# Kernel tuning notes

Hardware: AMD Instinct MI355X
Metric: run time of the kernel (lower is better)

Reference implementation:

```python
import jax, jax.numpy as jnp
import numpy as np

B, L, V, D = 8, 1024, 64, 64  # num_vars == d_model required by the module's g*h broadcast
EPS = 1e-5


def _layer_norm(x, gamma, beta):
    mu = jnp.mean(x, axis=-1, keepdims=True)
    var = jnp.mean(jnp.square(x - mu), axis=-1, keepdims=True)
    return (x - mu) * jax.lax.rsqrt(var + EPS) * gamma + beta


def setup_inputs() -> dict:
    key = jax.random.key(0)
    ks = jax.random.split(key, 20)
    s = 0.05
    inp = {
        'x': jax.random.normal(ks[0], (B, L, V), jnp.float32),
        # per-variable GRN(1, D, D) params, batched over V
        'W1': jax.random.normal(ks[1], (V, D), jnp.float32) * s,   # lin1 weight [in=1 -> D]
        'b1': jax.random.normal(ks[2], (V, D), jnp.float32) * s,
        'W2': jax.random.normal(ks[3], (V, D, D), jnp.float32) * s,
        'b2': jax.random.normal(ks[4], (V, D), jnp.float32) * s,
        'Wg': jax.random.normal(ks[5], (V, D, D), jnp.float32) * s,
        'bg': jax.random.normal(ks[6], (V, D), jnp.float32) * s,
        'Wsk': jax.random.normal(ks[7], (V, D), jnp.float32) * s,  # skip Linear(1, D)
        'bsk': jax.random.normal(ks[8], (V, D), jnp.float32) * s,
        'gamma': jnp.ones((V, D), jnp.float32),
        'beta': jnp.zeros((V, D), jnp.float32),
        # weight_net GRN(V*D, D, V) params
        'Wn1': jax.random.normal(ks[9], (V * D, D), jnp.float32) * s,
        'bn1': jax.random.normal(ks[10], (D,), jnp.float32) * s,
        'Wn2': jax.random.normal(ks[11], (D, D), jnp.float32) * s,
        'bn2': jax.random.normal(ks[12], (D,), jnp.float32) * s,
        'Wng': jax.random.normal(ks[13], (D, V), jnp.float32) * s,
        'bng': jax.random.normal(ks[14], (V,), jnp.float32) * s,
        'Wns': jax.random.normal(ks[15], (V * D, V), jnp.float32) * s,
        'bns': jax.random.normal(ks[16], (V,), jnp.float32) * s,
        'ngamma': jnp.ones((V,), jnp.float32),
        'nbeta': jnp.zeros((V,), jnp.float32),
    }
    return inp


def reference(x, W1, b1, W2, b2, Wg, bg, Wsk, bsk, gamma, beta,
              Wn1, bn1, Wn2, bn2, Wng, bng, Wns, bns, ngamma, nbeta):
    Bx, Lx, Vx = x.shape
    # --- per-variable GRN(1, D, D), batched over the variable axis ---
    h1 = jax.nn.elu(x[..., None] * W1 + b1)                      # [B,L,V,D]
    h2 = jnp.einsum('blvd,vde->blve', h1, W2) + b2               # [B,L,V,D]
    g = jax.nn.sigmoid(jnp.einsum('blvd,vde->blve', h2, Wg) + bg)
    skip = x[..., None] * Wsk + bsk                              # [B,L,V,D]
    stacked = _layer_norm(skip + g * h2, gamma, beta)            # [B,L,V,D]
    # --- weight net GRN(V*D, D, V) + softmax (note: requires V == D) ---
    flat = stacked.reshape(Bx, Lx, Vx * stacked.shape[-1])
    hw = jax.nn.elu(flat @ Wn1 + bn1)                            # [B,L,D]
    hw = hw @ Wn2 + bn2                                          # [B,L,D]
    gw = jax.nn.sigmoid(hw @ Wng + bng)                          # [B,L,V]
    skw = flat @ Wns + bns                                       # [B,L,V]
    weights = jax.nn.softmax(_layer_norm(skw + gw * hw, ngamma, nbeta), axis=-1)
    return jnp.einsum('blv,blvd->bld', weights, stacked)
```

## Files before the change

kernel.cpp:

```cpp
#include <hip/hip_runtime.h>
#include <hip/hip_bf16.h>
#include <math.h>

#define NV 64
#define ND 64
#define NTOK 8192
#define LN_EPS 1e-5f
#define KSPLIT 8
#define KRANGE (4096 / KSPLIT)

typedef __attribute__((ext_vector_type(8))) short s8v;
typedef __attribute__((ext_vector_type(4))) float f4v;
typedef __attribute__((ext_vector_type(4))) int   i4v;

__device__ __forceinline__ float sigm_f(float x) { return 1.f / (1.f + __expf(-x)); }
__device__ __forceinline__ float elu_f(float x)  { return x > 0.f ? x : (__expf(x) - 1.f); }

__device__ __forceinline__ float bf16_to_f(unsigned short s) {
    union { unsigned int u; float f; } c; c.u = ((unsigned int)s) << 16;
    return c.f;
}
__device__ __forceinline__ unsigned short bf16_rn(float f) {
    union { float f; unsigned int u; } c; c.f = f;
    return (unsigned short)((c.u + 0x8000u) >> 16);
}

__global__ __launch_bounds__(256) void vsn_prepack(
    const float* __restrict__ W2, const float* __restrict__ Wg,
    const float* __restrict__ Wn1, const float* __restrict__ Wns,
    short* __restrict__ w2b, short* __restrict__ wgb,
    __hip_bfloat16* __restrict__ wct)
{
    __shared__ float T[64][65];
    const int b = blockIdx.x, t = threadIdx.x;

    if (b < 64) {
        const float* src = W2 + (size_t)b * 4096;
        short* dst = w2b + (size_t)b * 4096;
        #pragma unroll
        for (int pass = 0; pass < 2; ++pass) {
            #pragma unroll
            for (int i = 0; i < 16; ++i) {
                int id = i * 256 + t;
                T[id & 63][id >> 6] = src[id];
            }
            __syncthreads();
            #pragma unroll
            for (int i = 0; i < 16; ++i) {
                int id = i * 256 + t;
                dst[id] = (short)bf16_rn(T[id >> 6][id & 63]);
            }
            __syncthreads();
            src = Wg + (size_t)b * 4096;
            dst = wgb + (size_t)b * 4096;
        }
    } else {
        int tb = b - 64;
        int half = tb >> 6, kt = tb & 63;
        const float* src = (half == 0 ? Wn1 : Wns) + (size_t)(kt * 64) * 64;
        #pragma unroll
        for (int i = 0; i < 16; ++i) {
            int id = i * 256 + t;
            T[id & 63][id >> 6] = src[id];
        }
        __syncthreads();
        #pragma unroll
        for (int i = 0; i < 16; ++i) {
            int id = i * 256 + t;
            int n = id >> 6, r = id & 63;
            wct[(size_t)(half * 64 + n) * 4096 + kt * 64 + r] =
                __float2bfloat16(T[n][r]);
        }
    }
}

__global__ __launch_bounds__(256) void vsn_stage1(
    const float* __restrict__ x,
    const float* __restrict__ W1, const float* __restrict__ b1,
    const short* __restrict__ w2b, const short* __restrict__ wgb,
    const float* __restrict__ b2, const float* __restrict__ bg,
    const float* __restrict__ Wsk, const float* __restrict__ bsk,
    const float* __restrict__ gamma, const float* __restrict__ beta,
    __hip_bfloat16* __restrict__ stb)
{
    const int t = threadIdx.x;
    const int wave = t >> 6, lane = t & 63;
    const int m16 = lane & 15, quad = lane >> 4;
    const int tile0 = blockIdx.x * 32;
    const int v = blockIdx.y * 4 + wave;

    __shared__ float xs[4][32];
    __shared__ __align__(16) unsigned short h2s[4][32][72];

    if (lane < 32) xs[wave][lane] = x[(size_t)(tile0 + lane) * NV + v];

    s8v a[2][2];
    #pragma unroll
    for (int kt = 0; kt < 2; ++kt) {
        float w1k[8], b1k[8];
        *(float4*)&w1k[0] = *(const float4*)(W1 + v * 64 + kt * 32 + quad * 8);
        *(float4*)&w1k[4] = *(const float4*)(W1 + v * 64 + kt * 32 + quad * 8 + 4);
        *(float4*)&b1k[0] = *(const float4*)(b1 + v * 64 + kt * 32 + quad * 8);
        *(float4*)&b1k[4] = *(const float4*)(b1 + v * 64 + kt * 32 + quad * 8 + 4);
        #pragma unroll
        for (int mi = 0; mi < 2; ++mi) {
            float xv = xs[wave][mi * 16 + m16];
            float h[8];
            #pragma unroll
            for (int j = 0; j < 8; ++j) h[j] = elu_f(fmaf(xv, w1k[j], b1k[j]));
            i4v av;
            #pragma unroll
            for (int p = 0; p < 4; ++p) {
                unsigned int u0 = __float_as_uint(h[2 * p]);
                unsigned int u1 = __float_as_uint(h[2 * p + 1]);
                av[p] = (int)((u1 & 0xffff0000u) | (u0 >> 16));
            }
            a[mi][kt] = *(s8v*)&av;
        }
    }

    f4v hacc[2][4];
    #pragma unroll
    for (int mi = 0; mi < 2; ++mi)
        #pragma unroll
        for (int ni = 0; ni < 4; ++ni) hacc[mi][ni] = (f4v){0.f, 0.f, 0.f, 0.f};

    const size_t wb = (size_t)v * 4096;
    #pragma unroll
    for (int ni = 0; ni < 4; ++ni)
        #pragma unroll
        for (int kt = 0; kt < 2; ++kt) {
            s8v bh = *(const s8v*)(w2b + wb + (size_t)(ni * 16 + m16) * 64 + kt * 32 + quad * 8);
            #pragma unroll
            for (int mi = 0; mi < 2; ++mi)
                hacc[mi][ni] = __builtin_amdgcn_mfma_f32_16x16x32_bf16(a[mi][kt], bh, hacc[mi][ni], 0, 0, 0);
        }
    {
        float b2d[4];
        #pragma unroll
        for (int ni = 0; ni < 4; ++ni) b2d[ni] = b2[v * 64 + ni * 16 + m16];
        #pragma unroll
        for (int mi = 0; mi < 2; ++mi)
            #pragma unroll
            for (int ni = 0; ni < 4; ++ni)
                #pragma unroll
                for (int r = 0; r < 4; ++r) hacc[mi][ni][r] += b2d[ni];
    }

    #pragma unroll
    for (int mi = 0; mi < 2; ++mi)
        #pragma unroll
        for (int ni = 0; ni < 4; ++ni)
            #pragma unroll
            for (int r = 0; r < 4; ++r)
                h2s[wave][mi * 16 + quad * 4 + r][ni * 16 + m16] =
                    (unsigned short)(__float_as_uint(hacc[mi][ni][r]) >> 16);

    s8v c[2][2];
    #pragma unroll
    for (int mi = 0; mi < 2; ++mi)
        #pragma unroll
        for (int kt = 0; kt < 2; ++kt)
            c[mi][kt] = *(const s8v*)&h2s[wave][mi * 16 + m16][kt * 32 + quad * 8];

    f4v gacc[2][4];
    #pragma unroll
    for (int mi = 0; mi < 2; ++mi)
        #pragma unroll
        for (int ni = 0; ni < 4; ++ni) gacc[mi][ni] = (f4v){0.f, 0.f, 0.f, 0.f};
    #pragma unroll
    for (int ni = 0; ni < 4; ++ni)
        #pragma unroll
        for (int kt = 0; kt < 2; ++kt) {
            s8v bh = *(const s8v*)(wgb + wb + (size_t)(ni * 16 + m16) * 64 + kt * 32 + quad * 8);
            #pragma unroll
            for (int mi = 0; mi < 2; ++mi)
                gacc[mi][ni] = __builtin_amdgcn_mfma_f32_16x16x32_bf16(c[mi][kt], bh, gacc[mi][ni], 0, 0, 0);
        }

    {
        float bgd[4], wskd[4], bskd[4];
        #pragma unroll
        for (int ni = 0; ni < 4; ++ni) {
            int d = v * 64 + ni * 16 + m16;
            bgd[ni] = bg[d]; wskd[ni] = Wsk[d]; bskd[ni] = bsk[d];
        }
        float xtok[2][4];
        #pragma unroll
        for (int mi = 0; mi < 2; ++mi)
            #pragma unroll
            for (int r = 0; r < 4; ++r) xtok[mi][r] = xs[wave][mi * 16 + quad * 4 + r];
        #pragma unroll
        for (int mi = 0; mi < 2; ++mi)
            #pragma unroll
            for (int ni = 0; ni < 4; ++ni)
                #pragma unroll
                for (int r = 0; r < 4; ++r) {
                    float g = sigm_f(gacc[mi][ni][r] + bgd[ni]);
                    gacc[mi][ni][r] = fmaf(xtok[mi][r], wskd[ni], bskd[ni]) + g * hacc[mi][ni][r];
                }
    }

    {
        float gamd[4], betd[4];
        #pragma unroll
        for (int ni = 0; ni < 4; ++ni) {
            int d = v * 64 + ni * 16 + m16;
            gamd[ni] = gamma[d]; betd[ni] = beta[d];
        }
        #pragma unroll
        for (int mi = 0; mi < 2; ++mi)
            #pragma unroll
            for (int r = 0; r < 4; ++r) {
                float s0 = gacc[mi][0][r], s1 = gacc[mi][1][r], s2 = gacc[mi][2][r], s3 = gacc[mi][3][r];
                float sum = s0 + s1 + s2 + s3;
                float sq  = s0 * s0 + s1 * s1 + s2 * s2 + s3 * s3;
                #pragma unroll
                for (int m = 1; m < 16; m <<= 1) { sum += __shfl_xor(sum, m); sq += __shfl_xor(sq, m); }
                float mu  = sum * 0.015625f;
                float var = sq * 0.015625f - mu * mu;
                float rs  = rsqrtf(var + LN_EPS);
                size_t base = (size_t)(tile0 + mi * 16 + quad * 4 + r) * 4096 + (size_t)v * 64 + m16;
                #pragma unroll
                for (int ni = 0; ni < 4; ++ni)
                    stb[base + ni * 16] = __hip_bfloat16_raw{
                        bf16_rn((gacc[mi][ni][r] - mu) * rs * gamd[ni] + betd[ni])};
            }
    }
}

__global__ __launch_bounds__(512) void vsn_stage2a(
    const __hip_bfloat16* __restrict__ stb,
    const __hip_bfloat16* __restrict__ wct,
    float* __restrict__ part)
{
    const int t = threadIdx.x;
    const int wave = t >> 6, lane = t & 63;
    const int mtile = wave >> 2;
    const int n0 = (wave & 3) * 32;
    const int tok0 = blockIdx.x * 128 + mtile * 64;
    const int s = blockIdx.y;
    const int k0 = s * KRANGE;
    const int m16 = lane & 15, quad = lane >> 4;

    const short* A  = (const short*)stb;
    const short* Bw = (const short*)wct;

    f4v acc[4][2];
    #pragma unroll
    for (int i = 0; i < 4; ++i)
        #pragma unroll
        for (int j = 0; j < 2; ++j)
            acc[i][j] = (f4v){0.f, 0.f, 0.f, 0.f};

    const short* arow = A  + (size_t)(tok0 + m16) * 4096 + quad * 8;
    const short* brow = Bw + (size_t)(n0 + m16) * 4096 + quad * 8;

    for (int k = k0; k < k0 + KRANGE; k += 32) {
        s8v a[4], b[2];
        #pragma unroll
        for (int i = 0; i < 4; ++i)
            a[i] = *(const s8v*)(arow + (size_t)i * 16 * 4096 + k);
        #pragma unroll
        for (int j = 0; j < 2; ++j)
            b[j] = *(const s8v*)(brow + (size_t)j * 16 * 4096 + k);
        #pragma unroll
        for (int i = 0; i < 4; ++i)
            #pragma unroll
            for (int j = 0; j < 2; ++j)
                acc[i][j] = __builtin_amdgcn_mfma_f32_16x16x32_bf16(a[i], b[j], acc[i][j], 0, 0, 0);
    }

    #pragma unroll
    for (int i = 0; i < 4; ++i)
        #pragma unroll
        for (int j = 0; j < 2; ++j)
            #pragma unroll
            for (int r = 0; r < 4; ++r)
                part[((size_t)(tok0 + i * 16 + quad * 4 + r)) * (KSPLIT * 128)
                     + s * 128 + n0 + j * 16 + m16] = acc[i][j][r];
}

__global__ __launch_bounds__(256) void vsn_stage2b(
    const __hip_bfloat16* __restrict__ stb, const float* __restrict__ part,
    const float* __restrict__ bn1,
    const float* __restrict__ Wn2, const float* __restrict__ bn2,
    const float* __restrict__ Wng, const float* __restrict__ bng,
    const float* __restrict__ bns,
    const float* __restrict__ ngamma, const float* __restrict__ nbeta,
    float* __restrict__ out)
{
    const int t = threadIdx.x;
    const int tok0 = blockIdx.x * 8;
    const int lane = t & 63, wv = t >> 6;

    __shared__ __align__(16) float hw1_s[8][64];
    __shared__ __align__(16) float skw_s[8][64];
    __shared__ __align__(16) float hw2_s[8][64];
    __shared__ float s2_s[8][64];
    __shared__ float w_s[8][64];

    #pragma unroll
    for (int tk = 0; tk < 2; ++tk) {
        int tl = wv * 2 + tk;
        const float* pr = part + (size_t)(tok0 + tl) * (KSPLIT * 128)
                        + (lane >> 5) * 128 + (lane & 31) * 4;
        float4 a0 = *(const float4*)(pr);
        float4 a1 = *(const float4*)(pr + 256);
        float4 a2 = *(const float4*)(pr + 512);
        float4 a3 = *(const float4*)(pr + 768);
        float tv[4];
        tv[0] = a0.x + a1.x + a2.x + a3.x;
        tv[1] = a0.y + a1.y + a2.y + a3.y;
        tv[2] = a0.z + a1.z + a2.z + a3.z;
        tv[3] = a0.w + a1.w + a2.w + a3.w;
        #pragma unroll
        for (int c = 0; c < 4; ++c) tv[c] += __shfl_xor(tv[c], 32);
        if (lane < 16) {
            int j0 = lane * 4;
            float4 bb = *(const float4*)(bn1 + j0);
            hw1_s[tl][j0 + 0] = elu_f(tv[0] + bb.x);
            hw1_s[tl][j0 + 1] = elu_f(tv[1] + bb.y);
            hw1_s[tl][j0 + 2] = elu_f(tv[2] + bb.z);
            hw1_s[tl][j0 + 3] = elu_f(tv[3] + bb.w);
        } else if (lane < 32) {
            int j0 = (lane - 16) * 4;
            float4 bb = *(const float4*)(bns + j0);
            skw_s[tl][j0 + 0] = tv[0] + bb.x;
            skw_s[tl][j0 + 1] = tv[1] + bb.y;
            skw_s[tl][j0 + 2] = tv[2] + bb.z;
            skw_s[tl][j0 + 3] = tv[3] + bb.w;
        }
    }
    __syncthreads();

    #pragma unroll
    for (int i = 0; i < 2; ++i) {
        int oidx = i * 256 + t;
        int tt = oidx >> 6, jj = oidx & 63;
        float acc = bn2[jj];
        #pragma unroll
        for (int k4 = 0; k4 < 16; ++k4) {
            float4 h = *(const float4*)&hw1_s[tt][k4 * 4];
            acc += h.x * Wn2[(k4*4+0)*64+jj] + h.y * Wn2[(k4*4+1)*64+jj]
                 + h.z * Wn2[(k4*4+2)*64+jj] + h.w * Wn2[(k4*4+3)*64+jj];
        }
        hw2_s[tt][jj] = acc;
    }
    __syncthreads();

    #pragma unroll
    for (int i = 0; i < 2; ++i) {
        int oidx = i * 256 + t;
        int tt = oidx >> 6, vv = oidx & 63;
        float acc = bng[vv];
        #pragma unroll
        for (int k4 = 0; k4 < 16; ++k4) {
            float4 h = *(const float4*)&hw2_s[tt][k4 * 4];
            acc += h.x * Wng[(k4*4+0)*64+vv] + h.y * Wng[(k4*4+1)*64+vv]
                 + h.z * Wng[(k4*4+2)*64+vv] + h.w * Wng[(k4*4+3)*64+vv];
        }
        float gw = sigm_f(acc);
        s2_s[tt][vv] = skw_s[tt][vv] + gw * hw2_s[tt][vv];
    }
    __syncthreads();

    if (t < 128) {
        int tt = t >> 4, l = t & 15;
        float z[4]; float sum = 0.f, sq = 0.f;
        #pragma unroll
        for (int i = 0; i < 4; ++i) { z[i] = s2_s[tt][l + 16 * i]; sum += z[i]; sq += z[i] * z[i]; }
        #pragma unroll
        for (int m = 1; m < 16; m <<= 1) { sum += __shfl_xor(sum, m); sq += __shfl_xor(sq, m); }
        float mu  = sum * 0.015625f;
        float var = sq * 0.015625f - mu * mu;
        float rs  = rsqrtf(var + LN_EPS);
        float ln[4]; float mx = -1e30f;
        #pragma unroll
        for (int i = 0; i < 4; ++i) {
            ln[i] = (z[i] - mu) * rs * ngamma[l + 16 * i] + nbeta[l + 16 * i];
            mx = fmaxf(mx, ln[i]);
        }
        #pragma unroll
        for (int m = 1; m < 16; m <<= 1) mx = fmaxf(mx, __shfl_xor(mx, m));
        float es = 0.f; float ev[4];
        #pragma unroll
        for (int i = 0; i < 4; ++i) { ev[i] = __expf(ln[i] - mx); es += ev[i]; }
        #pragma unroll
        for (int m = 1; m < 16; m <<= 1) es += __shfl_xor(es, m);
        float inv = 1.f / es;
        #pragma unroll
        for (int i = 0; i < 4; ++i) w_s[tt][l + 16 * i] = ev[i] * inv;
    }
    __syncthreads();

    {
        const int vloc = lane >> 3, d8 = (lane & 7) * 8;
        const short* s0 = (const short*)stb + (size_t)(tok0 + wv * 2) * 4096 + d8;
        const short* s1 = s0 + 4096;
        float acc0[8], acc1[8];
        #pragma unroll
        for (int j = 0; j < 8; ++j) { acc0[j] = 0.f; acc1[j] = 0.f; }
        #pragma unroll
        for (int vc = 0; vc < 8; ++vc) {
            int v = vc * 8 + vloc;
            s8v r0 = *(const s8v*)(s0 + v * 64);
            s8v r1 = *(const s8v*)(s1 + v * 64);
            float w0 = w_s[wv * 2][v], w1 = w_s[wv * 2 + 1][v];
            #pragma unroll
            for (int j = 0; j < 8; ++j) {
                acc0[j] = fmaf(w0, bf16_to_f((unsigned short)r0[j]), acc0[j]);
                acc1[j] = fmaf(w1, bf16_to_f((unsigned short)r1[j]), acc1[j]);
            }
        }
        #pragma unroll
        for (int m = 8; m <= 32; m <<= 1)
            #pragma unroll
            for (int j = 0; j < 8; ++j) {
                acc0[j] += __shfl_xor(acc0[j], m);
                acc1[j] += __shfl_xor(acc1[j], m);
            }
        if (lane < 8) {
            float* op = out + (size_t)(tok0 + wv * 2) * 64 + lane * 8;
            *(float4*)op       = make_float4(acc0[0], acc0[1], acc0[2], acc0[3]);
            *(float4*)(op + 4) = make_float4(acc0[4], acc0[5], acc0[6], acc0[7]);
            op += 64;
            *(float4*)op       = make_float4(acc1[0], acc1[1], acc1[2], acc1[3]);
            *(float4*)(op + 4) = make_float4(acc1[4], acc1[5], acc1[6], acc1[7]);
        }
    }
}

extern "C" void kernel_launch(void* const* d_in, const int* in_sizes, int n_in,
                              void* d_out, int out_size, void* d_ws, size_t ws_size,
                              hipStream_t stream) {
    const float* x     = (const float*)d_in[0];
    const float* W1    = (const float*)d_in[1];
    const float* b1    = (const float*)d_in[2];
    const float* W2    = (const float*)d_in[3];
    const float* b2    = (const float*)d_in[4];
    const float* Wg    = (const float*)d_in[5];
    const float* bg    = (const float*)d_in[6];
    const float* Wsk   = (const float*)d_in[7];
    const float* bsk   = (const float*)d_in[8];
    const float* gamma = (const float*)d_in[9];
    const float* beta  = (const float*)d_in[10];
    const float* Wn1   = (const float*)d_in[11];
    const float* bn1   = (const float*)d_in[12];
    const float* Wn2   = (const float*)d_in[13];
    const float* bn2   = (const float*)d_in[14];
    const float* Wng   = (const float*)d_in[15];
    const float* bng   = (const float*)d_in[16];
    const float* Wns   = (const float*)d_in[17];
    const float* bns   = (const float*)d_in[18];
    const float* ngam  = (const float*)d_in[19];
    const float* nbet  = (const float*)d_in[20];

    char* ws = (char*)d_ws;
    __hip_bfloat16* stb = (__hip_bfloat16*)ws;
    __hip_bfloat16* wct = (__hip_bfloat16*)(ws + (64u << 20));
    float* part = (float*)(ws + (65u << 20));
    short* w2b = (short*)(ws + (97u << 20));
    short* wgb = w2b + 262144;
    float* outp = (float*)d_out;

    vsn_prepack<<<dim3(192), 256, 0, stream>>>(W2, Wg, Wn1, Wns, w2b, wgb, wct);
    vsn_stage1<<<dim3(NTOK / 32, 16), 256, 0, stream>>>(
        x, W1, b1, w2b, wgb, b2, bg, Wsk, bsk, gamma, beta, stb);
    vsn_stage2a<<<dim3(NTOK / 128, KSPLIT), 512, 0, stream>>>(stb, wct, part);
    vsn_stage2b<<<dim3(NTOK / 8), 256, 0, stream>>>(
        stb, part, bn1, Wn2, bn2, Wng, bng, bns, ngam, nbet, outp);
}
```

Baseline: 228.5 us.

## Pad intermediate row strides, loop stage1 over token tiles, prefetch stacked rows

Pads the row strides of the stacked bf16 activations, the transposed weight-net weights and the split-K partials to avoid power-of-two strides that cause channel and bank conflicts. Stage1 now processes four 32-token tiles per block, loading per-variable parameters once and reusing them across tiles, with a quarter as many blocks. Stage2b issues the stacked-row loads before the softmax phase so their latency overlaps that computation. The costs are extra workspace and more registers held across the softmax.

```diff
diff --git a/kernel.cpp b/kernel.cpp
--- a/kernel.cpp
+++ b/kernel.cpp
@@ -8,6 +8,9 @@
 #define LN_EPS 1e-5f
 #define KSPLIT 8
 #define KRANGE (4096 / KSPLIT)
+#define SROW 4160
+#define WROW 4160
+#define PROW 1056
 
 typedef __attribute__((ext_vector_type(8))) short s8v;
 typedef __attribute__((ext_vector_type(4))) float f4v;
@@ -29,7 +32,7 @@
     const float* __restrict__ W2, const float* __restrict__ Wg,
     const float* __restrict__ Wn1, const float* __restrict__ Wns,
     short* __restrict__ w2b, short* __restrict__ wgb,
-    __hip_bfloat16* __restrict__ wct)
+    short* __restrict__ wct)
 {
     __shared__ float T[64][65];
     const int b = blockIdx.x, t = threadIdx.x;
@@ -68,8 +71,7 @@
         for (int i = 0; i < 16; ++i) {
             int id = i * 256 + t;
             int n = id >> 6, r = id & 63;
-            wct[(size_t)(half * 64 + n) * 4096 + kt * 64 + r] =
-                __float2bfloat16(T[n][r]);
+            wct[(size_t)(half * 64 + n) * WROW + kt * 64 + r] = (short)bf16_rn(T[n][r]);
         }
     }
 }
@@ -81,133 +83,126 @@
     const float* __restrict__ b2, const float* __restrict__ bg,
     const float* __restrict__ Wsk, const float* __restrict__ bsk,
     const float* __restrict__ gamma, const float* __restrict__ beta,
-    __hip_bfloat16* __restrict__ stb)
+    unsigned short* __restrict__ stb)
 {
     const int t = threadIdx.x;
     const int wave = t >> 6, lane = t & 63;
     const int m16 = lane & 15, quad = lane >> 4;
-    const int tile0 = blockIdx.x * 32;
     const int v = blockIdx.y * 4 + wave;
 
     __shared__ float xs[4][32];
     __shared__ __align__(16) unsigned short h2s[4][32][72];
 
-    if (lane < 32) xs[wave][lane] = x[(size_t)(tile0 + lane) * NV + v];
-
-    s8v a[2][2];
+    float w1k[2][8], b1k[2][8];
     #pragma unroll
     for (int kt = 0; kt < 2; ++kt) {
-        float w1k[8], b1k[8];
-        *(float4*)&w1k[0] = *(const float4*)(W1 + v * 64 + kt * 32 + quad * 8);
-        *(float4*)&w1k[4] = *(const float4*)(W1 + v * 64 + kt * 32 + quad * 8 + 4);
-        *(float4*)&b1k[0] = *(const float4*)(b1 + v * 64 + kt * 32 + quad * 8);
-        *(float4*)&b1k[4] = *(const float4*)(b1 + v * 64 + kt * 32 + quad * 8 + 4);
-        #pragma unroll
-        for (int mi = 0; mi < 2; ++mi) {
-            float xv = xs[wave][mi * 16 + m16];
-            float h[8];
-            #pragma unroll
-            for (int j = 0; j < 8; ++j) h[j] = elu_f(fmaf(xv, w1k[j], b1k[j]));
-            i4v av;
-            #pragma unroll
-            for (int p = 0; p < 4; ++p) {
-                unsigned int u0 = __float_as_uint(h[2 * p]);
-                unsigned int u1 = __float_as_uint(h[2 * p + 1]);
-                av[p] = (int)((u1 & 0xffff0000u) | (u0 >> 16));
-            }
-            a[mi][kt] = *(s8v*)&av;
-        }
-    }
-
-    f4v hacc[2][4];
-    #pragma unroll
-    for (int mi = 0; mi < 2; ++mi)
-        #pragma unroll
-        for (int ni = 0; ni < 4; ++ni) hacc[mi][ni] = (f4v){0.f, 0.f, 0.f, 0.f};
-
+        *(float4*)&w1k[kt][0] = *(const float4*)(W1 + v * 64 + kt * 32 + quad * 8);
+        *(float4*)&w1k[kt][4] = *(const float4*)(W1 + v * 64 + kt * 32 + quad * 8 + 4);
+        *(float4*)&b1k[kt][0] = *(const float4*)(b1 + v * 64 + kt * 32 + quad * 8);
+        *(float4*)&b1k[kt][4] = *(const float4*)(b1 + v * 64 + kt * 32 + quad * 8 + 4);
+    }
+    float b2d[4], bgd[4], wskd[4], bskd[4], gamd[4], betd[4];
+    #pragma unroll
+    for (int ni = 0; ni < 4; ++ni) {
+        int d = v * 64 + ni * 16 + m16;
+        b2d[ni] = b2[d]; bgd[ni] = bg[d]; wskd[ni] = Wsk[d]; bskd[ni] = bsk[d];
+        gamd[ni] = gamma[d]; betd[ni] = beta[d];
+    }
     const size_t wb = (size_t)v * 4096;
-    #pragma unroll
-    for (int ni = 0; ni < 4; ++ni)
-        #pragma unroll
-        for (int kt = 0; kt < 2; ++kt) {
-            s8v bh = *(const s8v*)(w2b + wb + (size_t)(ni * 16 + m16) * 64 + kt * 32 + quad * 8);
+
+    for (int tt4 = 0; tt4 < 4; ++tt4) {
+        const int tile0 = blockIdx.x * 128 + tt4 * 32;
+
+        if (lane < 32) xs[wave][lane] = x[(size_t)(tile0 + lane) * NV + v];
+
+        s8v a[2][2];
+        #pragma unroll
+        for (int kt = 0; kt < 2; ++kt)
+            #pragma unroll
+            for (int mi = 0; mi < 2; ++mi) {
+                float xv = xs[wave][mi * 16 + m16];
+                float h[8];
+                #pragma unroll
+                for (int j = 0; j < 8; ++j) h[j] = elu_f(fmaf(xv, w1k[kt][j], b1k[kt][j]));
+                i4v av;
+                #pragma unroll
+                for (int p = 0; p < 4; ++p) {
+                    unsigned int u0 = __float_as_uint(h[2 * p]);
+                    unsigned int u1 = __float_as_uint(h[2 * p + 1]);
+                    av[p] = (int)((u1 & 0xffff0000u) | (u0 >> 16));
+                }
+                a[mi][kt] = *(s8v*)&av;
+            }
+
+        f4v hacc[2][4];
+        #pragma unroll
+        for (int mi = 0; mi < 2; ++mi)
+            #pragma unroll
+            for (int ni = 0; ni < 4; ++ni) hacc[mi][ni] = (f4v){0.f, 0.f, 0.f, 0.f};
+        #pragma unroll
+        for (int ni = 0; ni < 4; ++ni)
+            #pragma unroll
+            for (int kt = 0; kt < 2; ++kt) {
+                s8v bh = *(const s8v*)(w2b + wb + (size_t)(ni * 16 + m16) * 64 + kt * 32 + quad * 8);
+                #pragma unroll
+                for (int mi = 0; mi < 2; ++mi)
+                    hacc[mi][ni] = __builtin_amdgcn_mfma_f32_16x16x32_bf16(a[mi][kt], bh, hacc[mi][ni], 0, 0, 0);
+            }
+        #pragma unroll
+        for (int mi = 0; mi < 2; ++mi)
+            #pragma unroll
+            for (int ni = 0; ni < 4; ++ni)
+                #pragma unroll
+                for (int r = 0; r < 4; ++r) hacc[mi][ni][r] += b2d[ni];
+
+        #pragma unroll
+        for (int mi = 0; mi < 2; ++mi)
+            #pragma unroll
+            for (int ni = 0; ni < 4; ++ni)
+                #pragma unroll
+                for (int r = 0; r < 4; ++r)
+                    h2s[wave][mi * 16 + quad * 4 + r][ni * 16 + m16] =
+                        (unsigned short)(__float_as_uint(hacc[mi][ni][r]) >> 16);
+
+        s8v c[2][2];
+        #pragma unroll
+        for (int mi = 0; mi < 2; ++mi)
+            #pragma unroll
+            for (int kt = 0; kt < 2; ++kt)
+                c[mi][kt] = *(const s8v*)&h2s[wave][mi * 16 + m16][kt * 32 + quad * 8];
+
+        f4v gacc[2][4];
+        #pragma unroll
+        for (int mi = 0; mi < 2; ++mi)
+            #pragma unroll
+            for (int ni = 0; ni < 4; ++ni) gacc[mi][ni] = (f4v){0.f, 0.f, 0.f, 0.f};
+        #pragma unroll
+        for (int ni = 0; ni < 4; ++ni)
+            #pragma unroll
+            for (int kt = 0; kt < 2; ++kt) {
+                s8v bh = *(const s8v*)(wgb + wb + (size_t)(ni * 16 + m16) * 64 + kt * 32 + quad * 8);
+                #pragma unroll
+                for (int mi = 0; mi < 2; ++mi)
+                    gacc[mi][ni] = __builtin_amdgcn_mfma_f32_16x16x32_bf16(c[mi][kt], bh, gacc[mi][ni], 0, 0, 0);
+            }
+
+        {
+            float xtok[2][4];
             #pragma unroll
             for (int mi = 0; mi < 2; ++mi)
-                hacc[mi][ni] = __builtin_amdgcn_mfma_f32_16x16x32_bf16(a[mi][kt], bh, hacc[mi][ni], 0, 0, 0);
-        }
-    {
-        float b2d[4];
-        #pragma unroll
-        for (int ni = 0; ni < 4; ++ni) b2d[ni] = b2[v * 64 + ni * 16 + m16];
-        #pragma unroll
-        for (int mi = 0; mi < 2; ++mi)
-            #pragma unroll
-            for (int ni = 0; ni < 4; ++ni)
-                #pragma unroll
-                for (int r = 0; r < 4; ++r) hacc[mi][ni][r] += b2d[ni];
-    }
-
-    #pragma unroll
-    for (int mi = 0; mi < 2; ++mi)
-        #pragma unroll
-        for (int ni = 0; ni < 4; ++ni)
-            #pragma unroll
-            for (int r = 0; r < 4; ++r)
-                h2s[wave][mi * 16 + quad * 4 + r][ni * 16 + m16] =
-                    (unsigned short)(__float_as_uint(hacc[mi][ni][r]) >> 16);
-
-    s8v c[2][2];
-    #pragma unroll
-    for (int mi = 0; mi < 2; ++mi)
-        #pragma unroll
-        for (int kt = 0; kt < 2; ++kt)
-            c[mi][kt] = *(const s8v*)&h2s[wave][mi * 16 + m16][kt * 32 + quad * 8];
-
-    f4v gacc[2][4];
-    #pragma unroll
-    for (int mi = 0; mi < 2; ++mi)
-        #pragma unroll
-        for (int ni = 0; ni < 4; ++ni) gacc[mi][ni] = (f4v){0.f, 0.f, 0.f, 0.f};
-    #pragma unroll
-    for (int ni = 0; ni < 4; ++ni)
-        #pragma unroll
-        for (int kt = 0; kt < 2; ++kt) {
-            s8v bh = *(const s8v*)(wgb + wb + (size_t)(ni * 16 + m16) * 64 + kt * 32 + quad * 8);
+                #pragma unroll
+                for (int r = 0; r < 4; ++r) xtok[mi][r] = xs[wave][mi * 16 + quad * 4 + r];
             #pragma unroll
             for (int mi = 0; mi < 2; ++mi)
-                gacc[mi][ni] = __builtin_amdgcn_mfma_f32_16x16x32_bf16(c[mi][kt], bh, gacc[mi][ni], 0, 0, 0);
-        }
-
-    {
-        float bgd[4], wskd[4], bskd[4];
-        #pragma unroll
-        for (int ni = 0; ni < 4; ++ni) {
-            int d = v * 64 + ni * 16 + m16;
-            bgd[ni] = bg[d]; wskd[ni] = Wsk[d]; bskd[ni] = bsk[d];
-        }
-        float xtok[2][4];
-        #pragma unroll
-        for (int mi = 0; mi < 2; ++mi)
-            #pragma unroll
-            for (int r = 0; r < 4; ++r) xtok[mi][r] = xs[wave][mi * 16 + quad * 4 + r];
-        #pragma unroll
-        for (int mi = 0; mi < 2; ++mi)
-            #pragma unroll
-            for (int ni = 0; ni < 4; ++ni)
-                #pragma unroll
-                for (int r = 0; r < 4; ++r) {
-                    float g = sigm_f(gacc[mi][ni][r] + bgd[ni]);
-                    gacc[mi][ni][r] = fmaf(xtok[mi][r], wskd[ni], bskd[ni]) + g * hacc[mi][ni][r];
-                }
-    }
-
-    {
-        float gamd[4], betd[4];
-        #pragma unroll
-        for (int ni = 0; ni < 4; ++ni) {
-            int d = v * 64 + ni * 16 + m16;
-            gamd[ni] = gamma[d]; betd[ni] = beta[d];
-        }
+                #pragma unroll
+                for (int ni = 0; ni < 4; ++ni)
+                    #pragma unroll
+                    for (int r = 0; r < 4; ++r) {
+                        float g = sigm_f(gacc[mi][ni][r] + bgd[ni]);
+                        gacc[mi][ni][r] = fmaf(xtok[mi][r], wskd[ni], bskd[ni]) + g * hacc[mi][ni][r];
+                    }
+        }
+
         #pragma unroll
         for (int mi = 0; mi < 2; ++mi)
             #pragma unroll
@@ -220,18 +215,18 @@
                 float mu  = sum * 0.015625f;
                 float var = sq * 0.015625f - mu * mu;
                 float rs  = rsqrtf(var + LN_EPS);
-                size_t base = (size_t)(tile0 + mi * 16 + quad * 4 + r) * 4096 + (size_t)v * 64 + m16;
+                size_t base = (size_t)(tile0 + mi * 16 + quad * 4 + r) * SROW + (size_t)v * 64 + m16;
                 #pragma unroll
                 for (int ni = 0; ni < 4; ++ni)
-                    stb[base + ni * 16] = __hip_bfloat16_raw{
-                        bf16_rn((gacc[mi][ni][r] - mu) * rs * gamd[ni] + betd[ni])};
+                    stb[base + ni * 16] =
+                        bf16_rn((gacc[mi][ni][r] - mu) * rs * gamd[ni] + betd[ni]);
             }
     }
 }
 
 __global__ __launch_bounds__(512) void vsn_stage2a(
-    const __hip_bfloat16* __restrict__ stb,
-    const __hip_bfloat16* __restrict__ wct,
+    const unsigned short* __restrict__ stb,
+    const short* __restrict__ wct,
     float* __restrict__ part)
 {
     const int t = threadIdx.x;
@@ -243,8 +238,7 @@
     const int k0 = s * KRANGE;
     const int m16 = lane & 15, quad = lane >> 4;
 
-    const short* A  = (const short*)stb;
-    const short* Bw = (const short*)wct;
+    const short* A = (const short*)stb;
 
     f4v acc[4][2];
     #pragma unroll
@@ -253,17 +247,17 @@
         for (int j = 0; j < 2; ++j)
             acc[i][j] = (f4v){0.f, 0.f, 0.f, 0.f};
 
-    const short* arow = A  + (size_t)(tok0 + m16) * 4096 + quad * 8;
-    const short* brow = Bw + (size_t)(n0 + m16) * 4096 + quad * 8;
+    const short* arow = A   + (size_t)(tok0 + m16) * SROW + quad * 8;
+    const short* brow = wct + (size_t)(n0 + m16) * WROW + quad * 8;
 
     for (int k = k0; k < k0 + KRANGE; k += 32) {
         s8v a[4], b[2];
         #pragma unroll
         for (int i = 0; i < 4; ++i)
-            a[i] = *(const s8v*)(arow + (size_t)i * 16 * 4096 + k);
+            a[i] = *(const s8v*)(arow + (size_t)i * 16 * SROW + k);
         #pragma unroll
         for (int j = 0; j < 2; ++j)
-            b[j] = *(const s8v*)(brow + (size_t)j * 16 * 4096 + k);
+            b[j] = *(const s8v*)(brow + (size_t)j * 16 * WROW + k);
         #pragma unroll
         for (int i = 0; i < 4; ++i)
             #pragma unroll
@@ -277,12 +271,12 @@
         for (int j = 0; j < 2; ++j)
             #pragma unroll
             for (int r = 0; r < 4; ++r)
-                part[((size_t)(tok0 + i * 16 + quad * 4 + r)) * (KSPLIT * 128)
+                part[(size_t)(tok0 + i * 16 + quad * 4 + r) * PROW
                      + s * 128 + n0 + j * 16 + m16] = acc[i][j][r];
 }
 
 __global__ __launch_bounds__(256) void vsn_stage2b(
-    const __hip_bfloat16* __restrict__ stb, const float* __restrict__ part,
+    const unsigned short* __restrict__ stb, const float* __restrict__ part,
     const float* __restrict__ bn1,
     const float* __restrict__ Wn2, const float* __restrict__ bn2,
     const float* __restrict__ Wng, const float* __restrict__ bng,
@@ -303,17 +297,14 @@
     #pragma unroll
     for (int tk = 0; tk < 2; ++tk) {
         int tl = wv * 2 + tk;
-        const float* pr = part + (size_t)(tok0 + tl) * (KSPLIT * 128)
+        const float* pr = part + (size_t)(tok0 + tl) * PROW
                         + (lane >> 5) * 128 + (lane & 31) * 4;
-        float4 a0 = *(const float4*)(pr);
-        float4 a1 = *(const float4*)(pr + 256);
-        float4 a2 = *(const float4*)(pr + 512);
-        float4 a3 = *(const float4*)(pr + 768);
-        float tv[4];
-        tv[0] = a0.x + a1.x + a2.x + a3.x;
-        tv[1] = a0.y + a1.y + a2.y + a3.y;
-        tv[2] = a0.z + a1.z + a2.z + a3.z;
-        tv[3] = a0.w + a1.w + a2.w + a3.w;
+        float tv[4] = {0.f, 0.f, 0.f, 0.f};
+        #pragma unroll
+        for (int i = 0; i < 4; ++i) {
+            float4 a = *(const float4*)(pr + i * 256);
+            tv[0] += a.x; tv[1] += a.y; tv[2] += a.z; tv[3] += a.w;
+        }
         #pragma unroll
         for (int c = 0; c < 4; ++c) tv[c] += __shfl_xor(tv[c], 32);
         if (lane < 16) {
@@ -365,6 +356,18 @@
     }
     __syncthreads();
 
+    const int vloc = lane >> 3, d8 = (lane & 7) * 8;
+    s8v r0[8], r1[8];
+    {
+        const short* s0 = (const short*)stb + (size_t)(tok0 + wv * 2) * SROW + d8;
+        const short* s1 = s0 + SROW;
+        #pragma unroll
+        for (int vc = 0; vc < 8; ++vc) {
+            r0[vc] = *(const s8v*)(s0 + (vc * 8 + vloc) * 64);
+            r1[vc] = *(const s8v*)(s1 + (vc * 8 + vloc) * 64);
+        }
+    }
+
     if (t < 128) {
         int tt = t >> 4, l = t & 15;
         float z[4]; float sum = 0.f, sq = 0.f;
@@ -395,22 +398,17 @@
     __syncthreads();
 
     {
-        const int vloc = lane >> 3, d8 = (lane & 7) * 8;
-        const short* s0 = (const short*)stb + (size_t)(tok0 + wv * 2) * 4096 + d8;
-        const short* s1 = s0 + 4096;
         float acc0[8], acc1[8];
         #pragma unroll
         for (int j = 0; j < 8; ++j) { acc0[j] = 0.f; acc1[j] = 0.f; }
         #pragma unroll
         for (int vc = 0; vc < 8; ++vc) {
             int v = vc * 8 + vloc;
-            s8v r0 = *(const s8v*)(s0 + v * 64);
-            s8v r1 = *(const s8v*)(s1 + v * 64);
             float w0 = w_s[wv * 2][v], w1 = w_s[wv * 2 + 1][v];
             #pragma unroll
             for (int j = 0; j < 8; ++j) {
-                acc0[j] = fmaf(w0, bf16_to_f((unsigned short)r0[j]), acc0[j]);
-                acc1[j] = fmaf(w1, bf16_to_f((unsigned short)r1[j]), acc1[j]);
+                acc0[j] = fmaf(w0, bf16_to_f((unsigned short)r0[vc][j]), acc0[j]);
+                acc1[j] = fmaf(w1, bf16_to_f((unsigned short)r1[vc][j]), acc1[j]);
             }
         }
         #pragma unroll
@@ -457,15 +455,15 @@
     const float* nbet  = (const float*)d_in[20];
 
     char* ws = (char*)d_ws;
-    __hip_bfloat16* stb = (__hip_bfloat16*)ws;
-    __hip_bfloat16* wct = (__hip_bfloat16*)(ws + (64u << 20));
-    float* part = (float*)(ws + (65u << 20));
-    short* w2b = (short*)(ws + (97u << 20));
+    unsigned short* stb = (unsigned short*)ws;
+    short* wct = (short*)(ws + (70u << 20));
+    float* part = (float*)(ws + (72u << 20));
+    short* w2b = (short*)(ws + (108u << 20));
     short* wgb = w2b + 262144;
     float* outp = (float*)d_out;
 
     vsn_prepack<<<dim3(192), 256, 0, stream>>>(W2, Wg, Wn1, Wns, w2b, wgb, wct);
-    vsn_stage1<<<dim3(NTOK / 32, 16), 256, 0, stream>>>(
+    vsn_stage1<<<dim3(NTOK / 128, 16), 256, 0, stream>>>(
         x, W1, b1, w2b, wgb, b2, bg, Wsk, bsk, gamma, beta, stb);
     vsn_stage2a<<<dim3(NTOK / 128, KSPLIT), 512, 0, stream>>>(stb, wct, part);
     vsn_stage2b<<<dim3(NTOK / 8), 256, 0, stream>>>(
```

Measured after the change: 222.8 us. -2.5%, faster.
